# Optimization experiments

Measured on AMD Instinct MI355X. Metric: run time of the kernel, lower is better.

## Reference

```python
import jax, jax.numpy as jnp
import numpy as np

N, E, F, H, C, G = 100000, 1000000, 64, 64, 10, 256


def setup_inputs() -> dict:
    key = jax.random.key(0)
    ks = jax.random.split(key, 16)
    s = 1.0 / np.sqrt(F)
    sh = 1.0 / np.sqrt(H)
    return {
        "x": jax.random.normal(ks[0], (N, F), dtype=jnp.float32),
        "edge_index": jax.random.randint(ks[1], (2, E), 0, N, dtype=jnp.int32),
        "edge_attr": jax.random.uniform(ks[2], (E,), dtype=jnp.float32),
        "batch": jnp.sort(jax.random.randint(ks[3], (N,), 0, G, dtype=jnp.int32)),
        "W1r": jax.random.uniform(ks[4], (F, H), minval=-s, maxval=s),
        "W1s": jax.random.uniform(ks[5], (F, H), minval=-s, maxval=s),
        "b1": jax.random.uniform(ks[6], (H,), minval=-s, maxval=s),
        "W2r": jax.random.uniform(ks[7], (H, H), minval=-sh, maxval=sh),
        "W2s": jax.random.uniform(ks[8], (H, H), minval=-sh, maxval=sh),
        "b2": jax.random.uniform(ks[9], (H,), minval=-sh, maxval=sh),
        "W3r": jax.random.uniform(ks[10], (H, H), minval=-sh, maxval=sh),
        "W3s": jax.random.uniform(ks[11], (H, H), minval=-sh, maxval=sh),
        "b3": jax.random.uniform(ks[12], (H,), minval=-sh, maxval=sh),
        "Wl": jax.random.uniform(ks[13], (H, C), minval=-sh, maxval=sh),
        "bl": jax.random.uniform(ks[14], (C,), minval=-sh, maxval=sh),
    }


def graph_conv(x, src, dst, ew, W_rel, W_root, b):
    # gather neighbor feats, weight per-edge, scatter-add to destination
    msgs = x[src] * ew[:, None]                              # [E, F]
    agg = jax.ops.segment_sum(msgs, dst, num_segments=N)     # [N, F]
    return agg @ W_rel + x @ W_root + b                      # [N, H]


def reference(x, edge_index, edge_attr, batch,
              W1r, W1s, b1, W2r, W2s, b2, W3r, W3s, b3, Wl, bl):
    src, dst = edge_index[0], edge_index[1]
    h = jax.nn.relu(graph_conv(x, src, dst, edge_attr, W1r, W1s, b1))
    h = jax.nn.relu(graph_conv(h, src, dst, edge_attr, W2r, W2s, b2))
    h = jax.nn.relu(graph_conv(h, src, dst, edge_attr, W3r, W3s, b3))
    # global mean pool over graphs in the batch
    sums = jax.ops.segment_sum(h, batch, num_segments=G)      # [G, H]
    cnts = jax.ops.segment_sum(jnp.ones((N,), h.dtype), batch, num_segments=G)
    pooled = sums / jnp.maximum(cnts, 1.0)[:, None]
    # dropout is identity in eval mode
    return pooled @ Wl + bl                                   # [G, C]
```

## Files before the change

### kernel.cpp

```cpp
#include <hip/hip_runtime.h>


#define GCN_F 64
#define GCN_C 10
#define CB_SHIFT 9
#define CB_NODES 512
#define NCB_MAX 200
#define CAP 7168
#define SC_CHUNK 2048

typedef __attribute__((ext_vector_type(8))) short bf16x8;
typedef __attribute__((ext_vector_type(4))) float f32x4;

__device__ __forceinline__ unsigned short f2b(float v) {
    union { float f; unsigned int u; } c; c.f = v;
    unsigned int u = c.u;
    return (unsigned short)((u + 0x7FFFu + ((u >> 16) & 1u)) >> 16);
}
__device__ __forceinline__ float b2f(unsigned short u) {
    union { unsigned int u; float f; } c; c.u = ((unsigned int)u) << 16; return c.f;
}

__global__ __launch_bounds__(256) void cvtz_kernel(const float* __restrict__ in,
                                                   unsigned short* __restrict__ out,
                                                   int n4, int* __restrict__ zp, int zn) {
    int gid = blockIdx.x * 256 + threadIdx.x;
    if (gid < zn) zp[gid] = 0;
    int stride = gridDim.x * 256;
    for (int i = gid; i < n4; i += stride) {
        float4 v = reinterpret_cast<const float4*>(in)[i];
        ushort4 o;
        o.x = f2b(v.x); o.y = f2b(v.y); o.z = f2b(v.z); o.w = f2b(v.w);
        reinterpret_cast<ushort4*>(out)[i] = o;
    }
}

__global__ __launch_bounds__(256) void scatterC_kernel(
    const int* __restrict__ src, const int* __restrict__ dst,
    const float* __restrict__ ew,
    int* __restrict__ gcursor, int2* __restrict__ ebufA, int E, int NCB) {
    __shared__ int2 recS[SC_CHUNK];
    __shared__ int gdest[SC_CHUNK];
    __shared__ int hist[NCB_MAX];
    __shared__ int lstart[NCB_MAX];
    __shared__ int gbase[NCB_MAX];
    __shared__ int cur[NCB_MAX];
    __shared__ int sb[256];

    int tid = threadIdx.x;
    int base = blockIdx.x * SC_CHUNK;
    int m = min(SC_CHUNK, E - base);

    for (int i = tid; i < NCB; i += 256) hist[i] = 0;
    __syncthreads();

    int2 rec[8];
    int bk[8];
#pragma unroll
    for (int k = 0; k < 8; ++k) {
        int e = base + k * 256 + tid;
        if (e < E) {
            int d = dst[e];
            bk[k] = d >> CB_SHIFT;
            rec[k] = make_int2(src[e] | ((d & (CB_NODES - 1)) << 17),
                               __float_as_int(ew[e]));
            atomicAdd(&hist[bk[k]], 1);
        } else bk[k] = -1;
    }
    __syncthreads();

    int v = (tid < NCB) ? hist[tid] : 0;
    sb[tid] = v;
    __syncthreads();
    for (int o = 1; o < 256; o <<= 1) {
        int t = (tid >= o) ? sb[tid - o] : 0;
        __syncthreads();
        sb[tid] += t;
        __syncthreads();
    }
    if (tid < NCB) {
        int excl = sb[tid] - v;
        lstart[tid] = excl;
        cur[tid] = excl;
        gbase[tid] = (v > 0) ? atomicAdd(&gcursor[tid], v) : 0;
    }
    __syncthreads();

#pragma unroll
    for (int k = 0; k < 8; ++k) {
        if (bk[k] >= 0) {
            int p = atomicAdd(&cur[bk[k]], 1);
            recS[p] = rec[k];
            gdest[p] = bk[k] * CAP + gbase[bk[k]] + (p - lstart[bk[k]]);
        }
    }
    __syncthreads();

    for (int i = tid; i < m; i += 256) ebufA[gdest[i]] = recS[i];
}

__global__ __launch_bounds__(256) void sortCB_kernel(
    const int2* __restrict__ ebufA, const int* __restrict__ gcursor,
    int2* __restrict__ ebufS, int* __restrict__ offsets, int* __restrict__ bend,
    int N, int E) {
    __shared__ int2 rec[CAP];
    __shared__ int cnt[CB_NODES];
    __shared__ int cur[CB_NODES];
    __shared__ int sbuf[256];
    int cb = blockIdx.x, tid = threadIdx.x;
    int e0 = cb * CAP;
    int m = min(gcursor[cb], CAP);
    if (tid == 0) bend[cb] = e0 + m;

    for (int i = tid; i < m; i += 256) rec[i] = ebufA[e0 + i];
    for (int i = tid; i < CB_NODES; i += 256) cnt[i] = 0;
    __syncthreads();
    for (int i = tid; i < m; i += 256)
        atomicAdd(&cnt[(unsigned)rec[i].x >> 17], 1);
    __syncthreads();

    int c0 = cnt[2 * tid], c1 = cnt[2 * tid + 1];
    int part = c0 + c1;
    sbuf[tid] = part;
    __syncthreads();
    for (int off = 1; off < 256; off <<= 1) {
        int t = (tid >= off) ? sbuf[tid - off] : 0;
        __syncthreads();
        sbuf[tid] += t;
        __syncthreads();
    }
    int excl = sbuf[tid] - part;
    int pre0 = excl, pre1 = excl + c0;
    cur[2 * tid] = pre0;
    cur[2 * tid + 1] = pre1;
    int g0 = cb * CB_NODES + 2 * tid;
    if (g0 <= N)     offsets[g0]     = e0 + pre0;
    if (g0 + 1 <= N) offsets[g0 + 1] = e0 + pre1;
    __syncthreads();

    for (int i = tid; i < m; i += 256) {
        int d9 = (unsigned)rec[i].x >> 17;
        int pos = atomicAdd(&cur[d9], 1);
        ebufS[e0 + pos] = make_int2(rec[i].x & 0x1FFFF, rec[i].y);
    }
}

__global__ __launch_bounds__(512) void layer_kernel(
    const unsigned short* __restrict__ xin, const int* __restrict__ offsets,
    const int* __restrict__ bend, const int2* __restrict__ ebufS,
    const float* __restrict__ Wr, const float* __restrict__ Ws,
    const float* __restrict__ b, unsigned short* __restrict__ out,
    int ngroups, int n)
{
    __shared__ __align__(16) unsigned short bfrag[2][2][4][64][8];
    __shared__ __align__(16) unsigned short aggS[8][16][72];
    int tid = threadIdx.x, lane = tid & 63, wave = tid >> 6;

    for (int i = tid; i < 8192; i += 512) {
        int op = i >> 12;
        int ks = (i >> 11) & 1;
        int ct = (i >> 9) & 3;
        int l  = (i >> 3) & 63;
        int j  = i & 7;
        int k   = ks * 32 + (l >> 4) * 8 + j;
        int col = ct * 16 + (l & 15);
        const float* W = op ? Ws : Wr;
        ((unsigned short*)bfrag)[i] = f2b(W[k * GCN_F + col]);
    }
    __syncthreads();

    int l8 = lane & 7;
    int grp = lane >> 3;
    int gbase = (lane & 56) << 2;
    int l15 = lane & 15, lhi = lane >> 4;

    bf16x8 B[2][2][4];
#pragma unroll
    for (int op = 0; op < 2; ++op)
#pragma unroll
        for (int ks = 0; ks < 2; ++ks)
#pragma unroll
            for (int ct = 0; ct < 4; ++ct)
                B[op][ks][ct] = *reinterpret_cast<const bf16x8*>(&bfrag[op][ks][ct][lane][0]);

    float bias[4];
#pragma unroll
    for (int ct = 0; ct < 4; ++ct) bias[ct] = b[ct * 16 + l15];

    int wid = blockIdx.x * 8 + wave;
    int nw  = gridDim.x * 8;
    for (int gsel = wid; gsel < ngroups; gsel += nw) {
        int wbase = gsel * 16;

#pragma unroll
        for (int half = 0; half < 2; ++half) {
            int node = wbase + half * 8 + grp;
            bool nv = node < n;
            int p0 = 0, p1 = 0;
            if (nv) {
                p0 = offsets[node];
                p1 = ((node & (CB_NODES - 1)) == CB_NODES - 1)
                         ? bend[node >> CB_SHIFT] : offsets[node + 1];
            }
            float acc[8] = {0.f, 0.f, 0.f, 0.f, 0.f, 0.f, 0.f, 0.f};

            int idx = p0 + l8;
            bool v = idx < p1;
            if (__any(v)) {
                int2 er = ebufS[v ? idx : 0];
                int s  = v ? er.x : 0;
                int wb = v ? er.y : 0;

                for (int c = 1;; ++c) {
                    int idxn = p0 + c * 8 + l8;
                    bool vn = idxn < p1;
                    int2 ern = ebufS[vn ? idxn : 0];

                    int sj[8], wj[8];
#pragma unroll
                    for (int j = 0; j < 8; ++j) {
                        sj[j] = __builtin_amdgcn_ds_bpermute(gbase + (j << 2), s);
                        wj[j] = __builtin_amdgcn_ds_bpermute(gbase + (j << 2), wb);
                    }
                    int4 r[8];
#pragma unroll
                    for (int j = 0; j < 8; ++j)
                        r[j] = *reinterpret_cast<const int4*>(
                            xin + ((size_t)sj[j] << 6) + l8 * 8);
#pragma unroll
                    for (int j = 0; j < 8; ++j) {
                        float wf = __int_as_float(wj[j]);
                        acc[0] = fmaf(__int_as_float(r[j].x << 16),        wf, acc[0]);
                        acc[1] = fmaf(__int_as_float(r[j].x & 0xFFFF0000), wf, acc[1]);
                        acc[2] = fmaf(__int_as_float(r[j].y << 16),        wf, acc[2]);
                        acc[3] = fmaf(__int_as_float(r[j].y & 0xFFFF0000), wf, acc[3]);
                        acc[4] = fmaf(__int_as_float(r[j].z << 16),        wf, acc[4]);
                        acc[5] = fmaf(__int_as_float(r[j].z & 0xFFFF0000), wf, acc[5]);
                        acc[6] = fmaf(__int_as_float(r[j].w << 16),        wf, acc[6]);
                        acc[7] = fmaf(__int_as_float(r[j].w & 0xFFFF0000), wf, acc[7]);
                    }

                    if (!__any(vn)) break;
                    s  = vn ? ern.x : 0;
                    wb = vn ? ern.y : 0;
                }
            }

            int4 o;
            o.x = (int)f2b(acc[0]) | ((int)f2b(acc[1]) << 16);
            o.y = (int)f2b(acc[2]) | ((int)f2b(acc[3]) << 16);
            o.z = (int)f2b(acc[4]) | ((int)f2b(acc[5]) << 16);
            o.w = (int)f2b(acc[6]) | ((int)f2b(acc[7]) << 16);
            *reinterpret_cast<int4*>(&aggS[wave][half * 8 + grp][l8 * 8]) = o;
        }

        bf16x8 a0 = *reinterpret_cast<const bf16x8*>(&aggS[wave][l15][lhi * 8]);
        bf16x8 a1 = *reinterpret_cast<const bf16x8*>(&aggS[wave][l15][32 + lhi * 8]);
        const unsigned short* xp = xin + (size_t)min(wbase + l15, n - 1) * GCN_F + lhi * 8;
        bf16x8 x0 = *reinterpret_cast<const bf16x8*>(xp);
        bf16x8 x1 = *reinterpret_cast<const bf16x8*>(xp + 32);

#pragma unroll
        for (int ct = 0; ct < 4; ++ct) {
            f32x4 acc = {0.f, 0.f, 0.f, 0.f};
            acc = __builtin_amdgcn_mfma_f32_16x16x32_bf16(a0, B[0][0][ct], acc, 0, 0, 0);
            acc = __builtin_amdgcn_mfma_f32_16x16x32_bf16(a1, B[0][1][ct], acc, 0, 0, 0);
            acc = __builtin_amdgcn_mfma_f32_16x16x32_bf16(x0, B[1][0][ct], acc, 0, 0, 0);
            acc = __builtin_amdgcn_mfma_f32_16x16x32_bf16(x1, B[1][1][ct], acc, 0, 0, 0);
            int col = ct * 16 + l15;
#pragma unroll
            for (int r = 0; r < 4; ++r) {
                int orow = wbase + lhi * 4 + r;
                if (orow < n) {
                    float v = fmaxf(acc[r] + bias[ct], 0.f);
                    out[(size_t)orow * GCN_F + col] = f2b(v);
                }
            }
        }
    }
}

__global__ __launch_bounds__(256) void pool_kernel(
    const unsigned short* __restrict__ h, const int* __restrict__ batch,
    const float* __restrict__ Wl, const float* __restrict__ bl,
    float* __restrict__ out, int n)
{
    int g    = blockIdx.x;
    int tid  = threadIdx.x;
    int lane = tid & 63;
    int wave = tid >> 6;

    int i0, i1;
    {
        int lo = 0, hi = n;
        while (lo < hi) { int mid = (lo + hi) >> 1; if (batch[mid] < g) lo = mid + 1; else hi = mid; }
        i0 = lo;
        lo = i0; hi = n;
        while (lo < hi) { int mid = (lo + hi) >> 1; if (batch[mid] < g + 1) lo = mid + 1; else hi = mid; }
        i1 = lo;
    }

    float s = 0.f;
    for (int i = i0 + wave; i < i1; i += 4) s += b2f(h[(size_t)i * GCN_F + lane]);

    __shared__ float sp[4][GCN_F];
    sp[wave][lane] = s;
    __syncthreads();
    if (wave == 0) {
        float tot = sp[0][lane] + sp[1][lane] + sp[2][lane] + sp[3][lane];
        float cntf = (float)(i1 - i0);
        sp[0][lane] = tot / fmaxf(cntf, 1.f);
    }
    __syncthreads();
    if (tid < GCN_C) {
        float o = bl[tid];
#pragma unroll
        for (int j = 0; j < GCN_F; ++j) o += sp[0][j] * Wl[j * GCN_C + tid];
        out[g * GCN_C + tid] = o;
    }
}

extern "C" void kernel_launch(void* const* d_in, const int* in_sizes, int n_in,
                              void* d_out, int out_size, void* d_ws, size_t ws_size,
                              hipStream_t stream) {
    const float* x     = (const float*)d_in[0];
    const int*   ei    = (const int*)d_in[1];
    const float* ew    = (const float*)d_in[2];
    const int*   batch = (const int*)d_in[3];
    const float* W1r   = (const float*)d_in[4];
    const float* W1s   = (const float*)d_in[5];
    const float* b1    = (const float*)d_in[6];
    const float* W2r   = (const float*)d_in[7];
    const float* W2s   = (const float*)d_in[8];
    const float* b2    = (const float*)d_in[9];
    const float* W3r   = (const float*)d_in[10];
    const float* W3s   = (const float*)d_in[11];
    const float* b3    = (const float*)d_in[12];
    const float* Wl    = (const float*)d_in[13];
    const float* bl    = (const float*)d_in[14];
    float* out = (float*)d_out;

    const int N = in_sizes[0] / GCN_F;
    const int E = in_sizes[2];
    const int G = out_size / GCN_C;
    const int NCB = (N + CB_NODES - 1) / CB_NODES;
    const int NGROUPS = (N + 15) / 16;

    const int* src = ei;
    const int* dst = ei + E;

    char* ws = (char*)d_ws;
    size_t off = 0;
    size_t csz = ((size_t)NCB * 4 + 15) & ~(size_t)15;
    int* gcursor = (int*)(ws + off);  off += csz;
    int* bend    = (int*)(ws + off);  off += csz;
    int* offsets = (int*)(ws + off);  off += ((size_t)(N + 1) * 4 + 15) & ~(size_t)15;
    int2* ebufA  = (int2*)(ws + off); off += (size_t)NCB * CAP * 8;
    int2* ebufS  = (int2*)(ws + off); off += (size_t)NCB * CAP * 8;
    unsigned short* buf0 = (unsigned short*)(ws + off); off += (size_t)N * GCN_F * 2;
    unsigned short* buf1 = (unsigned short*)(ws + off); off += (size_t)N * GCN_F * 2;

    int sblocks = (E + SC_CHUNK - 1) / SC_CHUNK;
    int zcount  = (int)(csz / 4);

    cvtz_kernel<<<1024, 256, 0, stream>>>(x, buf0, N * GCN_F / 4, gcursor, zcount);
    scatterC_kernel<<<sblocks, 256, 0, stream>>>(src, dst, ew, gcursor, ebufA, E, NCB);
    sortCB_kernel<<<NCB, 256, 0, stream>>>(ebufA, gcursor, ebufS, offsets, bend, N, E);

    const int LBLK = 512;
    layer_kernel<<<LBLK, 512, 0, stream>>>(buf0, offsets, bend, ebufS, W1r, W1s, b1,
                                           buf1, NGROUPS, N);
    layer_kernel<<<LBLK, 512, 0, stream>>>(buf1, offsets, bend, ebufS, W2r, W2s, b2,
                                           buf0, NGROUPS, N);
    layer_kernel<<<LBLK, 512, 0, stream>>>(buf0, offsets, bend, ebufS, W3r, W3s, b3,
                                           buf1, NGROUPS, N);

    pool_kernel<<<G, 256, 0, stream>>>(buf1, batch, Wl, bl, out, N);
}
```

Baseline: 211.4 us.

## Fuse three GraphConv layers and mean-pool into one cooperative kernel

Replaces the three layer launches and the pool launch with a single cooperative kernel that loops over the layers, separating them with grid-wide syncs, then runs the pooling and final linear layer. The aim is to remove kernel launch gaps and tail effects between the dependent stages. In exchange, the grid shrinks from 512 to 256 blocks, which halves the resident waves available to hide latency in the gather-heavy aggregation. It also adds grid-sync overhead, and the pool step assumes the grid size equals the number of graphs.

```diff
diff --git a/kernel.cpp b/kernel.cpp
--- a/kernel.cpp
+++ b/kernel.cpp
@@ -1,4 +1,7 @@
 #include <hip/hip_runtime.h>
+#include <hip/hip_cooperative_groups.h>
+
+namespace cg = cooperative_groups;
 
 
 #define GCN_F 64
@@ -145,178 +148,190 @@
     }
 }
 
-__global__ __launch_bounds__(512) void layer_kernel(
-    const unsigned short* __restrict__ xin, const int* __restrict__ offsets,
-    const int* __restrict__ bend, const int2* __restrict__ ebufS,
-    const float* __restrict__ Wr, const float* __restrict__ Ws,
-    const float* __restrict__ b, unsigned short* __restrict__ out,
+__global__ __launch_bounds__(512) void mega_kernel(
+    unsigned short* __restrict__ buf0, unsigned short* __restrict__ buf1,
+    const int* __restrict__ offsets, const int* __restrict__ bend,
+    const int2* __restrict__ ebufS,
+    const float* __restrict__ W1r, const float* __restrict__ W1s, const float* __restrict__ b1,
+    const float* __restrict__ W2r, const float* __restrict__ W2s, const float* __restrict__ b2,
+    const float* __restrict__ W3r, const float* __restrict__ W3s, const float* __restrict__ b3,
+    const float* __restrict__ Wl, const float* __restrict__ bl,
+    const int* __restrict__ batch, float* __restrict__ out,
     int ngroups, int n)
 {
+    cg::grid_group grid = cg::this_grid();
     __shared__ __align__(16) unsigned short bfrag[2][2][4][64][8];
     __shared__ __align__(16) unsigned short aggS[8][16][72];
+    __shared__ float sp[8][GCN_F];
+
     int tid = threadIdx.x, lane = tid & 63, wave = tid >> 6;
-
-    for (int i = tid; i < 8192; i += 512) {
-        int op = i >> 12;
-        int ks = (i >> 11) & 1;
-        int ct = (i >> 9) & 3;
-        int l  = (i >> 3) & 63;
-        int j  = i & 7;
-        int k   = ks * 32 + (l >> 4) * 8 + j;
-        int col = ct * 16 + (l & 15);
-        const float* W = op ? Ws : Wr;
-        ((unsigned short*)bfrag)[i] = f2b(W[k * GCN_F + col]);
-    }
-    __syncthreads();
-
     int l8 = lane & 7;
     int grp = lane >> 3;
     int gbase = (lane & 56) << 2;
     int l15 = lane & 15, lhi = lane >> 4;
 
-    bf16x8 B[2][2][4];
-#pragma unroll
-    for (int op = 0; op < 2; ++op)
-#pragma unroll
-        for (int ks = 0; ks < 2; ++ks)
-#pragma unroll
-            for (int ct = 0; ct < 4; ++ct)
-                B[op][ks][ct] = *reinterpret_cast<const bf16x8*>(&bfrag[op][ks][ct][lane][0]);
-
-    float bias[4];
-#pragma unroll
-    for (int ct = 0; ct < 4; ++ct) bias[ct] = b[ct * 16 + l15];
-
-    int wid = blockIdx.x * 8 + wave;
-    int nw  = gridDim.x * 8;
-    for (int gsel = wid; gsel < ngroups; gsel += nw) {
-        int wbase = gsel * 16;
-
-#pragma unroll
-        for (int half = 0; half < 2; ++half) {
-            int node = wbase + half * 8 + grp;
-            bool nv = node < n;
-            int p0 = 0, p1 = 0;
-            if (nv) {
-                p0 = offsets[node];
-                p1 = ((node & (CB_NODES - 1)) == CB_NODES - 1)
-                         ? bend[node >> CB_SHIFT] : offsets[node + 1];
+    for (int layer = 0; layer < 3; ++layer) {
+        if (layer) grid.sync();
+        const unsigned short* xin = (layer & 1) ? buf1 : buf0;
+        unsigned short* outb      = (layer & 1) ? buf0 : buf1;
+        const float* Wr = (layer == 0) ? W1r : (layer == 1) ? W2r : W3r;
+        const float* Ws = (layer == 0) ? W1s : (layer == 1) ? W2s : W3s;
+        const float* b  = (layer == 0) ? b1  : (layer == 1) ? b2  : b3;
+
+        for (int i = tid; i < 8192; i += 512) {
+            int op = i >> 12;
+            int ks = (i >> 11) & 1;
+            int ct = (i >> 9) & 3;
+            int l  = (i >> 3) & 63;
+            int j  = i & 7;
+            int k   = ks * 32 + (l >> 4) * 8 + j;
+            int col = ct * 16 + (l & 15);
+            const float* W = op ? Ws : Wr;
+            ((unsigned short*)bfrag)[i] = f2b(W[k * GCN_F + col]);
+        }
+        __syncthreads();
+
+        bf16x8 B[2][2][4];
+#pragma unroll
+        for (int op = 0; op < 2; ++op)
+#pragma unroll
+            for (int ks = 0; ks < 2; ++ks)
+#pragma unroll
+                for (int ct = 0; ct < 4; ++ct)
+                    B[op][ks][ct] = *reinterpret_cast<const bf16x8*>(&bfrag[op][ks][ct][lane][0]);
+
+        float bias[4];
+#pragma unroll
+        for (int ct = 0; ct < 4; ++ct) bias[ct] = b[ct * 16 + l15];
+
+        int wid = blockIdx.x * 8 + wave;
+        int nw  = gridDim.x * 8;
+        for (int gsel = wid; gsel < ngroups; gsel += nw) {
+            int wbase = gsel * 16;
+
+#pragma unroll
+            for (int half = 0; half < 2; ++half) {
+                int node = wbase + half * 8 + grp;
+                bool nv = node < n;
+                int p0 = 0, p1 = 0;
+                if (nv) {
+                    p0 = offsets[node];
+                    p1 = ((node & (CB_NODES - 1)) == CB_NODES - 1)
+                             ? bend[node >> CB_SHIFT] : offsets[node + 1];
+                }
+                float acc[8] = {0.f, 0.f, 0.f, 0.f, 0.f, 0.f, 0.f, 0.f};
+
+                int idx = p0 + l8;
+                bool v = idx < p1;
+                if (__any(v)) {
+                    int2 er = ebufS[v ? idx : 0];
+                    int s  = v ? er.x : 0;
+                    int wb = v ? er.y : 0;
+
+                    for (int c = 1;; ++c) {
+                        int idxn = p0 + c * 8 + l8;
+                        bool vn = idxn < p1;
+                        int2 ern = ebufS[vn ? idxn : 0];
+
+                        int sj[8], wj[8];
+#pragma unroll
+                        for (int j = 0; j < 8; ++j) {
+                            sj[j] = __builtin_amdgcn_ds_bpermute(gbase + (j << 2), s);
+                            wj[j] = __builtin_amdgcn_ds_bpermute(gbase + (j << 2), wb);
+                        }
+                        int4 r[8];
+#pragma unroll
+                        for (int j = 0; j < 8; ++j)
+                            r[j] = *reinterpret_cast<const int4*>(
+                                xin + ((size_t)sj[j] << 6) + l8 * 8);
+#pragma unroll
+                        for (int j = 0; j < 8; ++j) {
+                            float wf = __int_as_float(wj[j]);
+                            acc[0] = fmaf(__int_as_float(r[j].x << 16),        wf, acc[0]);
+                            acc[1] = fmaf(__int_as_float(r[j].x & 0xFFFF0000), wf, acc[1]);
+                            acc[2] = fmaf(__int_as_float(r[j].y << 16),        wf, acc[2]);
+                            acc[3] = fmaf(__int_as_float(r[j].y & 0xFFFF0000), wf, acc[3]);
+                            acc[4] = fmaf(__int_as_float(r[j].z << 16),        wf, acc[4]);
+                            acc[5] = fmaf(__int_as_float(r[j].z & 0xFFFF0000), wf, acc[5]);
+                            acc[6] = fmaf(__int_as_float(r[j].w << 16),        wf, acc[6]);
+                            acc[7] = fmaf(__int_as_float(r[j].w & 0xFFFF0000), wf, acc[7]);
+                        }
+
+                        if (!__any(vn)) break;
+                        s  = vn ? ern.x : 0;
+                        wb = vn ? ern.y : 0;
+                    }
+                }
+
+                int4 o;
+                o.x = (int)f2b(acc[0]) | ((int)f2b(acc[1]) << 16);
+                o.y = (int)f2b(acc[2]) | ((int)f2b(acc[3]) << 16);
+                o.z = (int)f2b(acc[4]) | ((int)f2b(acc[5]) << 16);
+                o.w = (int)f2b(acc[6]) | ((int)f2b(acc[7]) << 16);
+                *reinterpret_cast<int4*>(&aggS[wave][half * 8 + grp][l8 * 8]) = o;
             }
-            float acc[8] = {0.f, 0.f, 0.f, 0.f, 0.f, 0.f, 0.f, 0.f};
-
-            int idx = p0 + l8;
-            bool v = idx < p1;
-            if (__any(v)) {
-                int2 er = ebufS[v ? idx : 0];
-                int s  = v ? er.x : 0;
-                int wb = v ? er.y : 0;
-
-                for (int c = 1;; ++c) {
-                    int idxn = p0 + c * 8 + l8;
-                    bool vn = idxn < p1;
-                    int2 ern = ebufS[vn ? idxn : 0];
-
-                    int sj[8], wj[8];
-#pragma unroll
-                    for (int j = 0; j < 8; ++j) {
-                        sj[j] = __builtin_amdgcn_ds_bpermute(gbase + (j << 2), s);
-                        wj[j] = __builtin_amdgcn_ds_bpermute(gbase + (j << 2), wb);
+
+            bf16x8 a0 = *reinterpret_cast<const bf16x8*>(&aggS[wave][l15][lhi * 8]);
+            bf16x8 a1 = *reinterpret_cast<const bf16x8*>(&aggS[wave][l15][32 + lhi * 8]);
+            const unsigned short* xp = xin + (size_t)min(wbase + l15, n - 1) * GCN_F + lhi * 8;
+            bf16x8 x0 = *reinterpret_cast<const bf16x8*>(xp);
+            bf16x8 x1 = *reinterpret_cast<const bf16x8*>(xp + 32);
+
+#pragma unroll
+            for (int ct = 0; ct < 4; ++ct) {
+                f32x4 acc = {0.f, 0.f, 0.f, 0.f};
+                acc = __builtin_amdgcn_mfma_f32_16x16x32_bf16(a0, B[0][0][ct], acc, 0, 0, 0);
+                acc = __builtin_amdgcn_mfma_f32_16x16x32_bf16(a1, B[0][1][ct], acc, 0, 0, 0);
+                acc = __builtin_amdgcn_mfma_f32_16x16x32_bf16(x0, B[1][0][ct], acc, 0, 0, 0);
+                acc = __builtin_amdgcn_mfma_f32_16x16x32_bf16(x1, B[1][1][ct], acc, 0, 0, 0);
+                int col = ct * 16 + l15;
+#pragma unroll
+                for (int r = 0; r < 4; ++r) {
+                    int orow = wbase + lhi * 4 + r;
+                    if (orow < n) {
+                        float v = fmaxf(acc[r] + bias[ct], 0.f);
+                        outb[(size_t)orow * GCN_F + col] = f2b(v);
                     }
-                    int4 r[8];
-#pragma unroll
-                    for (int j = 0; j < 8; ++j)
-                        r[j] = *reinterpret_cast<const int4*>(
-                            xin + ((size_t)sj[j] << 6) + l8 * 8);
-#pragma unroll
-                    for (int j = 0; j < 8; ++j) {
-                        float wf = __int_as_float(wj[j]);
-                        acc[0] = fmaf(__int_as_float(r[j].x << 16),        wf, acc[0]);
-                        acc[1] = fmaf(__int_as_float(r[j].x & 0xFFFF0000), wf, acc[1]);
-                        acc[2] = fmaf(__int_as_float(r[j].y << 16),        wf, acc[2]);
-                        acc[3] = fmaf(__int_as_float(r[j].y & 0xFFFF0000), wf, acc[3]);
-                        acc[4] = fmaf(__int_as_float(r[j].z << 16),        wf, acc[4]);
-                        acc[5] = fmaf(__int_as_float(r[j].z & 0xFFFF0000), wf, acc[5]);
-                        acc[6] = fmaf(__int_as_float(r[j].w << 16),        wf, acc[6]);
-                        acc[7] = fmaf(__int_as_float(r[j].w & 0xFFFF0000), wf, acc[7]);
-                    }
-
-                    if (!__any(vn)) break;
-                    s  = vn ? ern.x : 0;
-                    wb = vn ? ern.y : 0;
                 }
             }
-
-            int4 o;
-            o.x = (int)f2b(acc[0]) | ((int)f2b(acc[1]) << 16);
-            o.y = (int)f2b(acc[2]) | ((int)f2b(acc[3]) << 16);
-            o.z = (int)f2b(acc[4]) | ((int)f2b(acc[5]) << 16);
-            o.w = (int)f2b(acc[6]) | ((int)f2b(acc[7]) << 16);
-            *reinterpret_cast<int4*>(&aggS[wave][half * 8 + grp][l8 * 8]) = o;
-        }
-
-        bf16x8 a0 = *reinterpret_cast<const bf16x8*>(&aggS[wave][l15][lhi * 8]);
-        bf16x8 a1 = *reinterpret_cast<const bf16x8*>(&aggS[wave][l15][32 + lhi * 8]);
-        const unsigned short* xp = xin + (size_t)min(wbase + l15, n - 1) * GCN_F + lhi * 8;
-        bf16x8 x0 = *reinterpret_cast<const bf16x8*>(xp);
-        bf16x8 x1 = *reinterpret_cast<const bf16x8*>(xp + 32);
-
-#pragma unroll
-        for (int ct = 0; ct < 4; ++ct) {
-            f32x4 acc = {0.f, 0.f, 0.f, 0.f};
-            acc = __builtin_amdgcn_mfma_f32_16x16x32_bf16(a0, B[0][0][ct], acc, 0, 0, 0);
-            acc = __builtin_amdgcn_mfma_f32_16x16x32_bf16(a1, B[0][1][ct], acc, 0, 0, 0);
-            acc = __builtin_amdgcn_mfma_f32_16x16x32_bf16(x0, B[1][0][ct], acc, 0, 0, 0);
-            acc = __builtin_amdgcn_mfma_f32_16x16x32_bf16(x1, B[1][1][ct], acc, 0, 0, 0);
-            int col = ct * 16 + l15;
-#pragma unroll
-            for (int r = 0; r < 4; ++r) {
-                int orow = wbase + lhi * 4 + r;
-                if (orow < n) {
-                    float v = fmaxf(acc[r] + bias[ct], 0.f);
-                    out[(size_t)orow * GCN_F + col] = f2b(v);
-                }
-            }
-        }
-    }
-}
-
-__global__ __launch_bounds__(256) void pool_kernel(
-    const unsigned short* __restrict__ h, const int* __restrict__ batch,
-    const float* __restrict__ Wl, const float* __restrict__ bl,
-    float* __restrict__ out, int n)
-{
-    int g    = blockIdx.x;
-    int tid  = threadIdx.x;
-    int lane = tid & 63;
-    int wave = tid >> 6;
-
-    int i0, i1;
+        }
+        __syncthreads();
+    }
+
+    grid.sync();
+
     {
-        int lo = 0, hi = n;
-        while (lo < hi) { int mid = (lo + hi) >> 1; if (batch[mid] < g) lo = mid + 1; else hi = mid; }
-        i0 = lo;
-        lo = i0; hi = n;
-        while (lo < hi) { int mid = (lo + hi) >> 1; if (batch[mid] < g + 1) lo = mid + 1; else hi = mid; }
-        i1 = lo;
-    }
-
-    float s = 0.f;
-    for (int i = i0 + wave; i < i1; i += 4) s += b2f(h[(size_t)i * GCN_F + lane]);
-
-    __shared__ float sp[4][GCN_F];
-    sp[wave][lane] = s;
-    __syncthreads();
-    if (wave == 0) {
-        float tot = sp[0][lane] + sp[1][lane] + sp[2][lane] + sp[3][lane];
-        float cntf = (float)(i1 - i0);
-        sp[0][lane] = tot / fmaxf(cntf, 1.f);
-    }
-    __syncthreads();
-    if (tid < GCN_C) {
-        float o = bl[tid];
-#pragma unroll
-        for (int j = 0; j < GCN_F; ++j) o += sp[0][j] * Wl[j * GCN_C + tid];
-        out[g * GCN_C + tid] = o;
+        const unsigned short* h = buf1;
+        int g = blockIdx.x;
+        int i0, i1;
+        {
+            int lo = 0, hi = n;
+            while (lo < hi) { int mid = (lo + hi) >> 1; if (batch[mid] < g) lo = mid + 1; else hi = mid; }
+            i0 = lo;
+            lo = i0; hi = n;
+            while (lo < hi) { int mid = (lo + hi) >> 1; if (batch[mid] < g + 1) lo = mid + 1; else hi = mid; }
+            i1 = lo;
+        }
+
+        float s = 0.f;
+        for (int i = i0 + wave; i < i1; i += 8) s += b2f(h[(size_t)i * GCN_F + lane]);
+
+        sp[wave][lane] = s;
+        __syncthreads();
+        if (wave == 0) {
+            float tot = 0.f;
+#pragma unroll
+            for (int w = 0; w < 8; ++w) tot += sp[w][lane];
+            float cntf = (float)(i1 - i0);
+            sp[0][lane] = tot / fmaxf(cntf, 1.f);
+        }
+        __syncthreads();
+        if (tid < GCN_C) {
+            float o = bl[tid];
+#pragma unroll
+            for (int j = 0; j < GCN_F; ++j) o += sp[0][j] * Wl[j * GCN_C + tid];
+            out[g * GCN_C + tid] = o;
+        }
     }
 }
 
@@ -344,7 +359,7 @@
     const int E = in_sizes[2];
     const int G = out_size / GCN_C;
     const int NCB = (N + CB_NODES - 1) / CB_NODES;
-    const int NGROUPS = (N + 15) / 16;
+    int NGROUPS = (N + 15) / 16;
 
     const int* src = ei;
     const int* dst = ei + E;
@@ -362,18 +377,20 @@
 
     int sblocks = (E + SC_CHUNK - 1) / SC_CHUNK;
     int zcount  = (int)(csz / 4);
+    int n = N;
 
     cvtz_kernel<<<1024, 256, 0, stream>>>(x, buf0, N * GCN_F / 4, gcursor, zcount);
     scatterC_kernel<<<sblocks, 256, 0, stream>>>(src, dst, ew, gcursor, ebufA, E, NCB);
     sortCB_kernel<<<NCB, 256, 0, stream>>>(ebufA, gcursor, ebufS, offsets, bend, N, E);
 
-    const int LBLK = 512;
-    layer_kernel<<<LBLK, 512, 0, stream>>>(buf0, offsets, bend, ebufS, W1r, W1s, b1,
-                                           buf1, NGROUPS, N);
-    layer_kernel<<<LBLK, 512, 0, stream>>>(buf1, offsets, bend, ebufS, W2r, W2s, b2,
-                                           buf0, NGROUPS, N);
-    layer_kernel<<<LBLK, 512, 0, stream>>>(buf0, offsets, bend, ebufS, W3r, W3s, b3,
-                                           buf1, NGROUPS, N);
-
-    pool_kernel<<<G, 256, 0, stream>>>(buf1, batch, Wl, bl, out, N);
-}
+    void* args[] = {
+        (void*)&buf0, (void*)&buf1, (void*)&offsets, (void*)&bend, (void*)&ebufS,
+        (void*)&W1r, (void*)&W1s, (void*)&b1,
+        (void*)&W2r, (void*)&W2s, (void*)&b2,
+        (void*)&W3r, (void*)&W3s, (void*)&b3,
+        (void*)&Wl, (void*)&bl, (void*)&batch, (void*)&out,
+        (void*)&NGROUPS, (void*)&n
+    };
+    hipLaunchCooperativeKernel((const void*)mega_kernel, dim3(256), dim3(512),
+                               args, 0, stream);
+}
```

New measurement: 320.1 us. 1.51x slower.
